# Kernel optimization log

Hardware: AMD Instinct MI355X
Metric: run time of the kernel (lower is better)

## Reference

```python
import math
import jax, jax.numpy as jnp
import numpy as np

WS = (8, 7, 7)   # window_size (d, h, w)
SS = (4, 3, 3)   # shift_size
NH = 4           # num_heads
DIM = 128


def _rel_position_index(ws):
    # [N*N] int index into the (2wd-1)(2wh-1)(2ww-1) bias table
    cd, ch, cw = np.arange(ws[0]), np.arange(ws[1]), np.arange(ws[2])
    coords = np.stack(np.meshgrid(cd, ch, cw, indexing='ij')).reshape(3, -1)  # [3, N]
    rel = (coords[:, :, None] - coords[:, None, :]).transpose(1, 2, 0)        # [N, N, 3]
    rel[..., 0] += ws[0] - 1
    rel[..., 1] += ws[1] - 1
    rel[..., 2] += ws[2] - 1
    rel[..., 0] *= (2 * ws[1] - 1) * (2 * ws[2] - 1)
    rel[..., 1] *= (2 * ws[2] - 1)
    return rel.sum(-1).reshape(-1)


def _rel_coords_table(ws):
    # [(2wd-1)(2wh-1)(2ww-1), 3] log-spaced continuous coords (Swin v2)
    rd = np.arange(-(ws[0] - 1), ws[0], dtype=np.float32)
    rh = np.arange(-(ws[1] - 1), ws[1], dtype=np.float32)
    rw = np.arange(-(ws[2] - 1), ws[2], dtype=np.float32)
    t = np.stack(np.meshgrid(rd, rh, rw, indexing='ij')).transpose(1, 2, 3, 0)  # [Td,Th,Tw,3]
    t[..., 0] /= ws[0] - 1
    t[..., 1] /= ws[1] - 1
    t[..., 2] /= ws[2] - 1
    t *= 8.0
    t = np.sign(t) * np.log2(np.abs(t) + 1.0) / 3.0
    return t.reshape(-1, 3)


_REL_INDEX = _rel_position_index(WS)
_COORDS = jnp.asarray(_rel_coords_table(WS))


def _attn_mask(pD, pH, pW, ws, ss):
    img = np.zeros((pD, pH, pW), np.float32)
    sl = lambda w, s: (slice(0, -w), slice(-w, -s), slice(-s, None))
    cnt = 0
    for d in sl(ws[0], ss[0]):
        for h in sl(ws[1], ss[1]):
            for w in sl(ws[2], ss[2]):
                img[d, h, w] = cnt
                cnt += 1
    m = img.reshape(pD // ws[0], ws[0], pH // ws[1], ws[1], pW // ws[2], ws[2])
    m = m.transpose(0, 2, 4, 1, 3, 5).reshape(-1, ws[0] * ws[1] * ws[2])  # [nWin, N]
    diff = m[:, None, :] - m[:, :, None]
    return jnp.asarray(np.where(diff != 0, -100.0, 0.0).astype(np.float32))


def setup_inputs() -> dict:
    key = jax.random.key(0)
    ks = jax.random.split(key, 6)
    B, D, H, W, C = 1, 16, 56, 56, DIM
    g = lambda k, shp, sc: jax.random.normal(k, shp, dtype=jnp.float32) * sc
    return {
        'x': g(ks[0], (B, D, H, W, C), 1.0),
        'qkv_weight': g(ks[1], (3 * C, C), 0.02),
        'qkv_bias': jnp.zeros((3 * C,), jnp.float32),
        'proj_weight': g(ks[2], (C, C), 0.02),
        'proj_bias': jnp.zeros((C,), jnp.float32),
        'logit_scale': jnp.full((NH, 1, 1), float(np.log(10.0)), jnp.float32),
        'cpb_w1': g(ks[3], (512, 3), 0.02),
        'cpb_b1': jnp.zeros((512,), jnp.float32),
        'cpb_w2': g(ks[4], (NH, 512), 0.02),
    }


def reference(x, qkv_weight, qkv_bias, proj_weight, proj_bias,
              logit_scale, cpb_w1, cpb_b1, cpb_w2):
    B, D, H, W, C = x.shape
    wd, wh, ww = WS
    hd = C // NH
    pad_d, pad_h, pad_w = (-D) % wd, (-H) % wh, (-W) % ww
    x = jnp.pad(x, ((0, 0), (0, pad_d), (0, pad_h), (0, pad_w), (0, 0)))
    pD, pH, pW = D + pad_d, H + pad_h, W + pad_w
    ss = [0 if WS[i] >= (pD, pH, pW)[i] else SS[i] for i in range(3)]
    shifted = sum(ss) > 0
    if shifted:
        x = jnp.roll(x, (-ss[0], -ss[1], -ss[2]), axis=(1, 2, 3))
    nd, nh, nw = pD // wd, pH // wh, pW // ww
    nWin, N = nd * nh * nw, wd * wh * ww
    # window partition -> [B*nWin, N, C]
    xw = x.reshape(B, nd, wd, nh, wh, nw, ww, C).transpose(0, 1, 3, 5, 2, 4, 6, 7)
    xw = xw.reshape(B * nWin, N, C)
    # qkv with k-bias zeroed (Swin v2 cosine attention)
    qb = qkv_bias.at[C:2 * C].set(0.0)
    qkv = (xw @ qkv_weight.T + qb).reshape(B * nWin, N, 3, NH, hd).transpose(2, 0, 3, 1, 4)
    q, k, v = qkv[0], qkv[1], qkv[2]   # each [B*nWin, NH, N, hd]
    qn = q / jnp.maximum(jnp.linalg.norm(q, axis=-1, keepdims=True), 1e-12)
    kn = k / jnp.maximum(jnp.linalg.norm(k, axis=-1, keepdims=True), 1e-12)
    attn = jnp.einsum('bhnd,bhmd->bhnm', qn, kn)
    scale = jnp.exp(jnp.minimum(logit_scale, math.log(100.0)))  # [NH,1,1]
    attn = attn * scale
    # continuous relative position bias
    table = jax.nn.relu(_COORDS @ cpb_w1.T + cpb_b1) @ cpb_w2.T  # [T, NH]
    bias = table[_REL_INDEX].reshape(N, N, NH).transpose(2, 0, 1)
    bias = 16.0 * jax.nn.sigmoid(bias)
    attn = attn + bias[None]
    if shifted:
        mask = _attn_mask(pD, pH, pW, WS, ss)  # [nWin, N, N]
        attn = attn.reshape(B, nWin, NH, N, N) + mask[None, :, None]
        attn = attn.reshape(B * nWin, NH, N, N)
    attn = jax.nn.softmax(attn, axis=-1)
    out = jnp.einsum('bhnm,bhmd->bhnd', attn, v).transpose(0, 2, 1, 3).reshape(B * nWin, N, C)
    out = out @ proj_weight.T + proj_bias
    # window reverse -> [B, pD, pH, pW, C]
    out = out.reshape(B, nd, nh, nw, wd, wh, ww, C).transpose(0, 1, 4, 2, 5, 3, 6, 7)
    out = out.reshape(B, pD, pH, pW, C)
    if shifted:
        out = jnp.roll(out, tuple(ss), axis=(1, 2, 3))
    return out[:, :D, :H, :W, :]
```

## Files before the change

kernel.cpp:

```cpp
#include <hip/hip_runtime.h>
#include <hip/hip_bf16.h>

typedef unsigned short u16;
typedef unsigned int   u32;
typedef float f32x4  __attribute__((ext_vector_type(4)));
typedef short bf16x8 __attribute__((ext_vector_type(8)));

#define DI __device__ __forceinline__

constexpr int TBL  = 2535;
constexpr int NTOK = 50176;

constexpr int WB_QW = 0;
constexpr int WB_PW = 49152;
constexpr int WB_QB = 65536;
constexpr int WB_PB = 65920;
constexpr int WB_TOT = 66048;

DI float b2f(u16 u){ return __uint_as_float(((u32)u)<<16); }
DI u16 f2b(float f){
  u32 u = __float_as_uint(f);
  return (u16)((u + 0x7fffu + ((u>>16)&1u)) >> 16);
}
DI float ldf(const void* p, int i, int isf32){
  return isf32 ? ((const float*)p)[i] : b2f(((const u16*)p)[i]);
}
DI f32x4 mfma16(bf16x8 a, bf16x8 b, f32x4 c){
  return __builtin_amdgcn_mfma_f32_16x16x32_bf16(a, b, c, 0, 0, 0);
}
DI u32 cvtpk(float lo, float hi){
  u32 r;
  asm("v_cvt_pk_bf16_f32 %0, %1, %2" : "=v"(r) : "v"(lo), "v"(hi));
  return r;
}
DI float ssq8(uint4 a){
  float s = 0.f, f;
  f=__uint_as_float(a.x<<16); s+=f*f; f=__uint_as_float(a.x&0xffff0000u); s+=f*f;
  f=__uint_as_float(a.y<<16); s+=f*f; f=__uint_as_float(a.y&0xffff0000u); s+=f*f;
  f=__uint_as_float(a.z<<16); s+=f*f; f=__uint_as_float(a.z&0xffff0000u); s+=f*f;
  f=__uint_as_float(a.w<<16); s+=f*f; f=__uint_as_float(a.w&0xffff0000u); s+=f*f;
  return s;
}

__global__ void k_detect(const u32* __restrict__ xw, int* __restrict__ flag){
  __shared__ int cnt;
  if (threadIdx.x == 0) cnt = 0;
  __syncthreads();
  int local = 0;
  for (int k = threadIdx.x; k < 4096; k += 256){
    u32 w = xw[k];
    u16 lo = (u16)w;
    u32 e = (lo >> 7) & 0xFF;
    if (lo != 0 && (e >= 143 || e <= 111)) local++;
  }
  atomicAdd(&cnt, local);
  __syncthreads();
  if (threadIdx.x == 0) *flag = (cnt > 1000) ? 1 : 0;
}

__global__ void k_wconv(const void* __restrict__ qw, const void* __restrict__ pw,
                        const void* __restrict__ qb, const void* __restrict__ pb,
                        const int* __restrict__ flag, u16* __restrict__ wb){
  const int isf32 = *flag;
  int i = blockIdx.x*256 + threadIdx.x;
  if (i >= WB_TOT) return;
  const void* src; int off;
  if (i < WB_PW)      { src = qw; off = i; }
  else if (i < WB_QB) { src = pw; off = i - WB_PW; }
  else if (i < WB_PB) { src = qb; off = i - WB_QB; }
  else                { src = pb; off = i - WB_PB; }
  wb[i] = isf32 ? f2b(((const float*)src)[off]) : ((const u16*)src)[off];
}

__global__ void k_cpb(const void* __restrict__ w1, const void* __restrict__ b1,
                      const void* __restrict__ w2, const int* __restrict__ flag,
                      float* __restrict__ table16){
  const int isf32 = *flag;
  int t = blockIdx.x, lane = threadIdx.x;
  int i = t/169; int r = t - i*169; int j = r/13; int k = r - j*13;
  float v0 = 8.f*(float)(i-7)/7.f, v1 = 8.f*(float)(j-6)/6.f, v2 = 8.f*(float)(k-6)/6.f;
  float c0 = copysignf(log2f(fabsf(v0)+1.f)*(1.f/3.f), v0);
  float c1 = copysignf(log2f(fabsf(v1)+1.f)*(1.f/3.f), v1);
  float c2 = copysignf(log2f(fabsf(v2)+1.f)*(1.f/3.f), v2);
  float a0=0.f,a1=0.f,a2=0.f,a3=0.f;
  for (int hh = lane; hh < 512; hh += 64){
    float a = c0*ldf(w1,hh*3,isf32) + c1*ldf(w1,hh*3+1,isf32)
            + c2*ldf(w1,hh*3+2,isf32) + ldf(b1,hh,isf32);
    a = fmaxf(a, 0.f);
    a0 += a*ldf(w2,hh,isf32);       a1 += a*ldf(w2,512+hh,isf32);
    a2 += a*ldf(w2,1024+hh,isf32);  a3 += a*ldf(w2,1536+hh,isf32);
  }
  #pragma unroll
  for (int off=32; off; off>>=1){
    a0 += __shfl_xor(a0, off); a1 += __shfl_xor(a1, off);
    a2 += __shfl_xor(a2, off); a3 += __shfl_xor(a3, off);
  }
  if (lane==0){
    table16[t]       = 16.f/(1.f+__expf(-a0));
    table16[TBL+t]   = 16.f/(1.f+__expf(-a1));
    table16[2*TBL+t] = 16.f/(1.f+__expf(-a2));
    table16[3*TBL+t] = 16.f/(1.f+__expf(-a3));
  }
}

__global__ void k_bias(const float* __restrict__ table16, float* __restrict__ bias16){
  int n = blockIdx.x, h = blockIdx.y;
  int td = n/49; int r2 = n - td*49; int th = r2/7; int tw = r2 - th*7;
  const float* tb = table16 + h*TBL;
  float* o = bias16 + ((size_t)h*392 + n)*392;
  for (int m = threadIdx.x; m < 392; m += 128){
    int sd = m/49; int q2 = m - sd*49; int sh = q2/7; int sw = q2 - sh*7;
    int idx = (td - sd + 7)*169 + (th - sh + 6)*13 + (tw - sw + 6);
    o[m] = tb[idx];
  }
}

__global__ __launch_bounds__(256,3) void k_qkv(const void* __restrict__ x,
    const u16* __restrict__ wb, const int* __restrict__ flag, u16* __restrict__ qkvbuf){
  __shared__ __align__(16) u16 As[64*136];
  __shared__ __align__(16) u16 Ws[128*136];
  const int isf32 = *flag;
  const int tid = threadIdx.x;
  const int tokbase0 = blockIdx.x*64;
  {
    int trow = tid>>2, cq = (tid&3)*32;
    int gtok = tokbase0 + trow;
    int win = gtok/392, tt = gtok - win*392;
    int dwi = win>>6, hwi = (win>>3)&7, wwi = win&7;
    int td = tt/49; int r2 = tt - td*49; int th = r2/7; int tw = r2 - th*7;
    int pd = dwi*8 + td + 4; if (pd >= 16) pd -= 16;
    int ph = hwi*7 + th + 3; if (ph >= 56) ph -= 56;
    int pw = wwi*7 + tw + 3; if (pw >= 56) pw -= 56;
    size_t pos = (size_t)((pd*56 + ph)*56 + pw)*128 + cq;
    if (isf32){
      const float4* src = (const float4*)((const float*)x + pos);
      #pragma unroll
      for (int u=0; u<8; ++u){
        float4 a = src[u];
        ushort4 s4 = make_ushort4(f2b(a.x), f2b(a.y), f2b(a.z), f2b(a.w));
        *(ushort4*)&As[trow*136 + cq + u*4] = s4;
      }
    } else {
      const uint4* src = (const uint4*)((const u16*)x + pos);
      #pragma unroll
      for (int u=0; u<4; ++u) *(uint4*)&As[trow*136 + cq + u*8] = src[u];
    }
  }
  const int wave = tid>>6, lane = tid&63;
  const int c = lane & 15, g = lane >> 4;
  const int tokbase = tokbase0 + wave*16;
  bf16x8 ka[4];
  for (int which = 0; which < 3; ++which){
    __syncthreads();
    {
      int orow = tid>>1, c2 = (tid&1)*64;
      const uint4* src = (const uint4*)(wb + WB_QW + (size_t)(which*128 + orow)*128 + c2);
      #pragma unroll
      for (int u=0; u<8; ++u) *(uint4*)&Ws[orow*136 + c2 + u*8] = src[u];
    }
    __syncthreads();
    if (which == 0){
      #pragma unroll
      for (int kk=0; kk<4; ++kk)
        ka[kk] = *(const bf16x8*)&As[(wave*16 + c)*136 + kk*32 + g*8];
    }
    f32x4 acc[8];
    #pragma unroll
    for (int nt=0; nt<8; ++nt) acc[nt] = 0.f;
    #pragma unroll
    for (int nt=0; nt<8; ++nt){
      #pragma unroll
      for (int kk=0; kk<4; ++kk){
        bf16x8 wf = *(const bf16x8*)&Ws[(nt*16 + c)*136 + kk*32 + g*8];
        acc[nt] = mfma16(ka[kk], wf, acc[nt]);
      }
    }
    #pragma unroll
    for (int nt=0; nt<8; ++nt){
      int oc = nt*16 + c;
      float bv = (which==1) ? 0.f : b2f(wb[WB_QB + which*128 + oc]);
      int head = oc >> 5, chb = oc & 31;
      #pragma unroll
      for (int r=0;r<4;++r){
        int t = tokbase + 4*g + r;
        qkvbuf[((size_t)(which*4+head)*NTOK + t)*32 + chb] = f2b(acc[nt][r] + bv);
      }
    }
  }
}

#define QKT_STEP(JT, JJ) do { \
  bf16x8 kf = *(const bf16x8*)&klds[((JT)*16 + c)*40 + g*8]; \
  f32x4 tz = {0.f,0.f,0.f,0.f}; \
  f32x4 t = mfma16(kf, qf, tz); \
  const int mb = (JT)*16 + 4*g; \
  const int mbc = (mb <= 388) ? mb : 388; \
  const float4 bq = *(const float4*)(brow + mbc); \
  const int4 cmq = *(const int4*)&cnt[mbc]; \
  float s0 = fmaf(t[0], qsc, bq.x + ((cmq.x==cn) ? -15.f : -115.f)); \
  float s1 = fmaf(t[1], qsc, bq.y + ((cmq.y==cn) ? -15.f : -115.f)); \
  float s2 = fmaf(t[2], qsc, bq.z + ((cmq.z==cn) ? -15.f : -115.f)); \
  float s3 = fmaf(t[3], qsc, bq.w + ((cmq.w==cn) ? -15.f : -115.f)); \
  float p0 = __expf(s0), p1 = __expf(s1), p2 = __expf(s2), p3 = __expf(s3); \
  if (mb > 388){ p0=0.f; p1=0.f; p2=0.f; p3=0.f; } \
  sum += (p0+p1) + (p2+p3); \
  uint2 wv; wv.x = cvtpk(p0,p1); wv.y = cvtpk(p2,p3); \
  *(uint2*)&psw[c*20 + (JJ)*8 + 2*g] = wv; \
} while(0)

#define PV_STEP(MC) do { \
  bf16x8 pf = *(const bf16x8*)&psw[c*20 + 4*g]; \
  bf16x8 va = *(const bf16x8*)&vT[c*424 + (MC)*32 + g*8]; \
  bf16x8 vb = *(const bf16x8*)&vT[(16+c)*424 + (MC)*32 + g*8]; \
  o0 = mfma16(va, pf, o0); \
  o1 = mfma16(vb, pf, o1); \
} while(0)

__global__ __launch_bounds__(512,4) void k_attn(const u16* __restrict__ qkv,
    const float* __restrict__ bias16, const void* __restrict__ lsc,
    const int* __restrict__ flag, u16* __restrict__ aout){
  __shared__ __align__(16) u16 klds[400*40];
  __shared__ __align__(16) u16 vT[32*424];
  __shared__ __align__(16) u32 ps[8][16*20];
  __shared__ __align__(16) float qs[400];
  __shared__ __align__(16) int   cnt[400];
  const int isf32 = *flag;
  const int tid = threadIdx.x;
  const int win = blockIdx.x, h = blockIdx.y;
  const int dwi = win>>6, hwi = (win>>3)&7, wwi = win&7;
  const u16* qg = qkv + ((size_t)(0*4 + h)*NTOK + (size_t)win*392)*32;
  const u16* kg = qkv + ((size_t)(1*4 + h)*NTOK + (size_t)win*392)*32;
  const u16* vg = qkv + ((size_t)(2*4 + h)*NTOK + (size_t)win*392)*32;
  const float ls = isf32 ? ((const float*)lsc)[h] : b2f(((const u16*)lsc)[h]);
  const float scale = __expf(fminf(ls, 4.60517019f));

  for (int idx = tid; idx < 800; idx += 512){
    const int row = idx>>1, half = idx&1;
    if (row < 392){
      const uint4* kp = (const uint4*)(kg + (size_t)row*32 + half*16);
      uint4 a = kp[0], b = kp[1];
      float fv[16];
      fv[0] =__uint_as_float(a.x<<16); fv[1] =__uint_as_float(a.x&0xffff0000u);
      fv[2] =__uint_as_float(a.y<<16); fv[3] =__uint_as_float(a.y&0xffff0000u);
      fv[4] =__uint_as_float(a.z<<16); fv[5] =__uint_as_float(a.z&0xffff0000u);
      fv[6] =__uint_as_float(a.w<<16); fv[7] =__uint_as_float(a.w&0xffff0000u);
      fv[8] =__uint_as_float(b.x<<16); fv[9] =__uint_as_float(b.x&0xffff0000u);
      fv[10]=__uint_as_float(b.y<<16); fv[11]=__uint_as_float(b.y&0xffff0000u);
      fv[12]=__uint_as_float(b.z<<16); fv[13]=__uint_as_float(b.z&0xffff0000u);
      fv[14]=__uint_as_float(b.w<<16); fv[15]=__uint_as_float(b.w&0xffff0000u);
      float ss = 0.f;
      #pragma unroll
      for (int e=0;e<16;++e) ss = fmaf(fv[e], fv[e], ss);
      ss += __shfl_xor(ss, 1);
      const float rn = 1.f/fmaxf(sqrtf(ss), 1e-12f);
      u16 ob[16];
      #pragma unroll
      for (int e=0;e<16;++e) ob[e] = f2b(fv[e]*rn);
      uint4 w0, w1;
      w0.x = (u32)ob[0] |((u32)ob[1] <<16); w0.y = (u32)ob[2] |((u32)ob[3] <<16);
      w0.z = (u32)ob[4] |((u32)ob[5] <<16); w0.w = (u32)ob[6] |((u32)ob[7] <<16);
      w1.x = (u32)ob[8] |((u32)ob[9] <<16); w1.y = (u32)ob[10]|((u32)ob[11]<<16);
      w1.z = (u32)ob[12]|((u32)ob[13]<<16); w1.w = (u32)ob[14]|((u32)ob[15]<<16);
      *(uint4*)&klds[row*40 + half*16]     = w0;
      *(uint4*)&klds[row*40 + half*16 + 8] = w1;
      const uint4* qp = (const uint4*)(qg + (size_t)row*32 + half*16);
      float sq = ssq8(qp[0]) + ssq8(qp[1]);
      sq += __shfl_xor(sq, 1);
      if (half == 0) qs[row] = scale / fmaxf(sqrtf(sq), 1e-12f);
    } else {
      uint4 z = {0,0,0,0};
      *(uint4*)&klds[row*40 + half*16]     = z;
      *(uint4*)&klds[row*40 + half*16 + 8] = z;
      if (half == 0) qs[row] = 1.f;
    }
  }
  for (int t2 = tid; t2 < 400; t2 += 512){
    int row = (t2 < 392) ? t2 : 391;
    int td = row/49; int r2 = row - td*49; int th = r2/7; int tw = r2 - th*7;
    int gd = dwi*8 + td, gh = hwi*7 + th, gw = wwi*7 + tw;
    int rd = (gd < 8) ? 0 : ((gd < 12) ? 1 : 2);
    int rh = (gh < 49) ? 0 : ((gh < 53) ? 1 : 2);
    int rw = (gw < 49) ? 0 : ((gw < 53) ? 1 : 2);
    cnt[t2] = rd*9 + rh*3 + rw;
  }
  for (int idx = tid; idx < 1568; idx += 512){
    int m = idx>>2, cq = idx&3;
    uint4 b = ((const uint4*)vg)[idx];
    int ch = cq*8;
    vT[(ch+0)*424 + m] = (u16)b.x;  vT[(ch+1)*424 + m] = (u16)(b.x>>16);
    vT[(ch+2)*424 + m] = (u16)b.y;  vT[(ch+3)*424 + m] = (u16)(b.y>>16);
    vT[(ch+4)*424 + m] = (u16)b.z;  vT[(ch+5)*424 + m] = (u16)(b.z>>16);
    vT[(ch+6)*424 + m] = (u16)b.w;  vT[(ch+7)*424 + m] = (u16)(b.w>>16);
  }
  for (int idx = tid; idx < 1024; idx += 512){
    int ch = idx>>5, mm = 392 + (idx&31);
    vT[ch*424 + mm] = 0;
  }
  __syncthreads();

  const int wave = tid>>6, lane = tid&63;
  const int c = lane & 15, g = lane >> 4;
  u32* psw = &ps[wave][0];
  for (int rt = wave; rt < 25; rt += 8){
    const int nb = rt*16;
    const int nc = (nb + c < 392) ? (nb + c) : 391;
    const bf16x8 qf = *(const bf16x8*)(qg + (size_t)nc*32 + g*8);
    const float qsc = qs[nc];
    const int   cn  = cnt[nc];
    const float* brow = bias16 + (size_t)h*153664 + (size_t)nc*392;
    float sum = 0.f;
    f32x4 o0 = {0.f,0.f,0.f,0.f}, o1 = {0.f,0.f,0.f,0.f};
    for (int mc = 0; mc < 12; ++mc){
      QKT_STEP(2*mc,   0);
      QKT_STEP(2*mc+1, 1);
      PV_STEP(mc);
    }
    QKT_STEP(24, 0);
    { uint2 zz; zz.x = 0u; zz.y = 0u; *(uint2*)&psw[c*20 + 8 + 2*g] = zz; }
    PV_STEP(12);
    sum += __shfl_xor(sum, 16);
    sum += __shfl_xor(sum, 32);
    const float rv = 1.f/sum;
    uint2 wa, wb2;
    wa.x  = cvtpk(o0[0]*rv, o0[1]*rv);  wa.y  = cvtpk(o0[2]*rv, o0[3]*rv);
    wb2.x = cvtpk(o1[0]*rv, o1[1]*rv);  wb2.y = cvtpk(o1[2]*rv, o1[3]*rv);
    *(uint2*)&psw[c*20 + 2*g]     = wa;
    *(uint2*)&psw[c*20 + 8 + 2*g] = wb2;
    const int orow = lane>>2, oq = lane&3;
    uint4 ov = *(const uint4*)&psw[orow*20 + 4*oq];
    const int n = nb + orow;
    if (n < 392)
      *(uint4*)(aout + ((size_t)(win*392 + n))*128 + h*32 + oq*8) = ov;
  }
}

__global__ __launch_bounds__(256,2) void k_proj(const u16* __restrict__ ain,
    const u16* __restrict__ wb, const int* __restrict__ flag, void* __restrict__ out){
  __shared__ __align__(16) u16 As[64*136];
  __shared__ __align__(16) u16 Ws[128*136];
  const int isf32 = *flag;
  const int tid = threadIdx.x;
  const int tokbase0 = blockIdx.x*64;
  {
    int trow = tid>>2, cq = (tid&3)*32;
    const uint4* src = (const uint4*)(ain + (size_t)(tokbase0+trow)*128 + cq);
    #pragma unroll
    for (int u=0; u<4; ++u) *(uint4*)&As[trow*136 + cq + u*8] = src[u];
  }
  {
    int orow = tid>>1, c2 = (tid&1)*64;
    const uint4* src = (const uint4*)(wb + WB_PW + (size_t)orow*128 + c2);
    #pragma unroll
    for (int u=0; u<8; ++u) *(uint4*)&Ws[orow*136 + c2 + u*8] = src[u];
  }
  __syncthreads();
  const int wave = tid>>6, lane = tid&63;
  const int c = lane & 15, g = lane >> 4;
  bf16x8 ka[4];
  #pragma unroll
  for (int kk=0; kk<4; ++kk)
    ka[kk] = *(const bf16x8*)&As[(wave*16 + c)*136 + kk*32 + g*8];
  f32x4 acc[8];
  #pragma unroll
  for (int nt=0; nt<8; ++nt) acc[nt] = 0.f;
  #pragma unroll
  for (int nt=0; nt<8; ++nt){
    #pragma unroll
    for (int kk=0; kk<4; ++kk){
      bf16x8 wf = *(const bf16x8*)&Ws[(nt*16 + c)*136 + kk*32 + g*8];
      acc[nt] = mfma16(ka[kk], wf, acc[nt]);
    }
  }
  const int tokbase = tokbase0 + wave*16;
  size_t po[4];
  #pragma unroll
  for (int r=0;r<4;++r){
    int gtok = tokbase + 4*g + r;
    int win = gtok/392, tt = gtok - win*392;
    int dwi = win>>6, hwi = (win>>3)&7, wwi = win&7;
    int td = tt/49; int r2 = tt - td*49; int th = r2/7; int tw = r2 - th*7;
    int pd = dwi*8 + td + 4; if (pd >= 16) pd -= 16;
    int ph = hwi*7 + th + 3; if (ph >= 56) ph -= 56;
    int pwx = wwi*7 + tw + 3; if (pwx >= 56) pwx -= 56;
    po[r] = (size_t)((pd*56 + ph)*56 + pwx)*128;
  }
  #pragma unroll
  for (int nt=0; nt<8; ++nt){
    int oc = nt*16 + c;
    float bv = b2f(wb[WB_PB + oc]);
    #pragma unroll
    for (int r=0;r<4;++r){
      float v = acc[nt][r] + bv;
      if (isf32) ((float*)out)[po[r] + oc] = v;
      else       ((u16*)out)[po[r] + oc] = f2b(v);
    }
  }
}

extern "C" void kernel_launch(void* const* d_in, const int* in_sizes, int n_in,
                              void* d_out, int out_size, void* d_ws, size_t ws_size,
                              hipStream_t stream){
  const void* x      = d_in[0];
  const void* qkv_w  = d_in[1];
  const void* qkv_b  = d_in[2];
  const void* proj_w = d_in[3];
  const void* proj_b = d_in[4];
  const void* lsc    = d_in[5];
  const void* cpb_w1 = d_in[6];
  const void* cpb_b1 = d_in[7];
  const void* cpb_w2 = d_in[8];
  char* ws = (char*)d_ws;
  int*   flag    = (int*)(ws);
  float* table16 = (float*)(ws + 256);
  float* bias16  = (float*)(ws + 41216);
  u16*   wb      = (u16*)(ws + 2499840);
  u16*   qkvbuf  = (u16*)(ws + 2631936);
  u16*   attnout = (u16*)(ws + 41167104);

  k_detect<<<1, 256, 0, stream>>>((const u32*)x, flag);
  k_wconv<<<(WB_TOT+255)/256, 256, 0, stream>>>(qkv_w, proj_w, qkv_b, proj_b, flag, wb);
  k_cpb <<<TBL, 64, 0, stream>>>(cpb_w1, cpb_b1, cpb_w2, flag, table16);
  k_bias<<<dim3(392,4), 128, 0, stream>>>(table16, bias16);
  k_qkv <<<784, 256, 0, stream>>>(x, wb, flag, qkvbuf);
  k_attn<<<dim3(128,4), 512, 0, stream>>>(qkvbuf, bias16, lsc, flag, attnout);
  k_proj<<<784, 256, 0, stream>>>(attnout, wb, flag, d_out);
}
```

Baseline: 102.6 us.

## Fuse q/k normalization into QKV GEMM, simplify attention softmax and merge weight conversion

Moves the L2 normalization of q and k, plus the logit scale, into the QKV projection epilogue, so the attention kernel no longer renormalizes K or computes q norms. The bias table is pre-shifted and pre-scaled by log2(e), which lets the inner loop use a raw v_exp_f32 with no multiply, and the mask is applied as a zeroing select only for windows that straddle shift regions. The row sum now comes from an extra MFMA against a vector of ones instead of shuffle reductions. Weight conversion is folded into the cpb kernel to remove one launch. The risks are extra shuffles in the QKV epilogue, one more MFMA per PV step, and rounding normalized q/k to bf16 before the dot product.

```diff
diff --git a/kernel.cpp b/kernel.cpp
--- a/kernel.cpp
+++ b/kernel.cpp
@@ -10,6 +10,7 @@
 
 constexpr int TBL  = 2535;
 constexpr int NTOK = 50176;
+constexpr float L2E = 1.4426950408889634f;
 
 constexpr int WB_QW = 0;
 constexpr int WB_PW = 49152;
@@ -33,13 +34,10 @@
   asm("v_cvt_pk_bf16_f32 %0, %1, %2" : "=v"(r) : "v"(lo), "v"(hi));
   return r;
 }
-DI float ssq8(uint4 a){
-  float s = 0.f, f;
-  f=__uint_as_float(a.x<<16); s+=f*f; f=__uint_as_float(a.x&0xffff0000u); s+=f*f;
-  f=__uint_as_float(a.y<<16); s+=f*f; f=__uint_as_float(a.y&0xffff0000u); s+=f*f;
-  f=__uint_as_float(a.z<<16); s+=f*f; f=__uint_as_float(a.z&0xffff0000u); s+=f*f;
-  f=__uint_as_float(a.w<<16); s+=f*f; f=__uint_as_float(a.w&0xffff0000u); s+=f*f;
-  return s;
+DI float vexp2(float x){
+  float r;
+  asm("v_exp_f32 %0, %1" : "=v"(r) : "v"(x));
+  return r;
 }
 
 __global__ void k_detect(const u32* __restrict__ xw, int* __restrict__ flag){
@@ -58,24 +56,23 @@
   if (threadIdx.x == 0) *flag = (cnt > 1000) ? 1 : 0;
 }
 
-__global__ void k_wconv(const void* __restrict__ qw, const void* __restrict__ pw,
-                        const void* __restrict__ qb, const void* __restrict__ pb,
-                        const int* __restrict__ flag, u16* __restrict__ wb){
-  const int isf32 = *flag;
-  int i = blockIdx.x*256 + threadIdx.x;
-  if (i >= WB_TOT) return;
-  const void* src; int off;
-  if (i < WB_PW)      { src = qw; off = i; }
-  else if (i < WB_QB) { src = pw; off = i - WB_PW; }
-  else if (i < WB_PB) { src = qb; off = i - WB_QB; }
-  else                { src = pb; off = i - WB_PB; }
-  wb[i] = isf32 ? f2b(((const float*)src)[off]) : ((const u16*)src)[off];
-}
-
 __global__ void k_cpb(const void* __restrict__ w1, const void* __restrict__ b1,
                       const void* __restrict__ w2, const int* __restrict__ flag,
-                      float* __restrict__ table16){
+                      const void* __restrict__ qw, const void* __restrict__ pw,
+                      const void* __restrict__ qb, const void* __restrict__ pb,
+                      u16* __restrict__ wb, float* __restrict__ table16){
   const int isf32 = *flag;
+  {
+    int gid = blockIdx.x*64 + threadIdx.x;
+    if (gid < WB_TOT){
+      const void* src; int off;
+      if (gid < WB_PW)      { src = qw; off = gid; }
+      else if (gid < WB_QB) { src = pw; off = gid - WB_PW; }
+      else if (gid < WB_PB) { src = qb; off = gid - WB_QB; }
+      else                  { src = pb; off = gid - WB_PB; }
+      wb[gid] = isf32 ? f2b(((const float*)src)[off]) : ((const u16*)src)[off];
+    }
+  }
   int t = blockIdx.x, lane = threadIdx.x;
   int i = t/169; int r = t - i*169; int j = r/13; int k = r - j*13;
   float v0 = 8.f*(float)(i-7)/7.f, v1 = 8.f*(float)(j-6)/6.f, v2 = 8.f*(float)(k-6)/6.f;
@@ -96,10 +93,10 @@
     a2 += __shfl_xor(a2, off); a3 += __shfl_xor(a3, off);
   }
   if (lane==0){
-    table16[t]       = 16.f/(1.f+__expf(-a0));
-    table16[TBL+t]   = 16.f/(1.f+__expf(-a1));
-    table16[2*TBL+t] = 16.f/(1.f+__expf(-a2));
-    table16[3*TBL+t] = 16.f/(1.f+__expf(-a3));
+    table16[t]       = (16.f/(1.f+__expf(-a0)) - 15.f)*L2E;
+    table16[TBL+t]   = (16.f/(1.f+__expf(-a1)) - 15.f)*L2E;
+    table16[2*TBL+t] = (16.f/(1.f+__expf(-a2)) - 15.f)*L2E;
+    table16[3*TBL+t] = (16.f/(1.f+__expf(-a3)) - 15.f)*L2E;
   }
 }
 
@@ -116,7 +113,8 @@
 }
 
 __global__ __launch_bounds__(256,3) void k_qkv(const void* __restrict__ x,
-    const u16* __restrict__ wb, const int* __restrict__ flag, u16* __restrict__ qkvbuf){
+    const u16* __restrict__ wb, const void* __restrict__ lsc,
+    const int* __restrict__ flag, u16* __restrict__ qkvbuf){
   __shared__ __align__(16) u16 As[64*136];
   __shared__ __align__(16) u16 Ws[128*136];
   const int isf32 = *flag;
@@ -149,6 +147,12 @@
   const int wave = tid>>6, lane = tid&63;
   const int c = lane & 15, g = lane >> 4;
   const int tokbase = tokbase0 + wave*16;
+  float sl2e[4];
+  #pragma unroll
+  for (int h2=0; h2<4; ++h2){
+    float ls = ldf(lsc, h2, isf32);
+    sl2e[h2] = __expf(fminf(ls, 4.60517019f)) * L2E;
+  }
   bf16x8 ka[4];
   for (int which = 0; which < 3; ++which){
     __syncthreads();
@@ -175,35 +179,67 @@
         acc[nt] = mfma16(ka[kk], wf, acc[nt]);
       }
     }
+    if (which != 1){
+      #pragma unroll
+      for (int nt=0; nt<8; ++nt){
+        float bv = b2f(wb[WB_QB + which*128 + nt*16 + c]);
+        #pragma unroll
+        for (int r=0;r<4;++r) acc[nt][r] += bv;
+      }
+    }
+    if (which < 2){
+      #pragma unroll
+      for (int h2=0; h2<4; ++h2){
+        f32x4 ss;
+        #pragma unroll
+        for (int r=0;r<4;++r)
+          ss[r] = acc[2*h2][r]*acc[2*h2][r] + acc[2*h2+1][r]*acc[2*h2+1][r];
+        #pragma unroll
+        for (int off=1; off<16; off<<=1){
+          #pragma unroll
+          for (int r=0;r<4;++r) ss[r] += __shfl_xor(ss[r], off);
+        }
+        #pragma unroll
+        for (int r=0;r<4;++r){
+          float rn = rsqrtf(fmaxf(ss[r], 1e-24f));
+          if (which == 0) rn *= sl2e[h2];
+          acc[2*h2][r]   *= rn;
+          acc[2*h2+1][r] *= rn;
+        }
+      }
+    }
     #pragma unroll
     for (int nt=0; nt<8; ++nt){
       int oc = nt*16 + c;
-      float bv = (which==1) ? 0.f : b2f(wb[WB_QB + which*128 + oc]);
       int head = oc >> 5, chb = oc & 31;
       #pragma unroll
       for (int r=0;r<4;++r){
         int t = tokbase + 4*g + r;
-        qkvbuf[((size_t)(which*4+head)*NTOK + t)*32 + chb] = f2b(acc[nt][r] + bv);
+        qkvbuf[((size_t)(which*4+head)*NTOK + t)*32 + chb] = f2b(acc[nt][r]);
       }
     }
   }
 }
 
-#define QKT_STEP(JT, JJ) do { \
+#define QKT_STEP(JT, JJ, TAIL, MIXED) do { \
   bf16x8 kf = *(const bf16x8*)&klds[((JT)*16 + c)*40 + g*8]; \
   f32x4 tz = {0.f,0.f,0.f,0.f}; \
   f32x4 t = mfma16(kf, qf, tz); \
   const int mb = (JT)*16 + 4*g; \
-  const int mbc = (mb <= 388) ? mb : 388; \
+  const int mbc = (TAIL) ? ((mb <= 388) ? mb : 388) : mb; \
   const float4 bq = *(const float4*)(brow + mbc); \
-  const int4 cmq = *(const int4*)&cnt[mbc]; \
-  float s0 = fmaf(t[0], qsc, bq.x + ((cmq.x==cn) ? -15.f : -115.f)); \
-  float s1 = fmaf(t[1], qsc, bq.y + ((cmq.y==cn) ? -15.f : -115.f)); \
-  float s2 = fmaf(t[2], qsc, bq.z + ((cmq.z==cn) ? -15.f : -115.f)); \
-  float s3 = fmaf(t[3], qsc, bq.w + ((cmq.w==cn) ? -15.f : -115.f)); \
-  float p0 = __expf(s0), p1 = __expf(s1), p2 = __expf(s2), p3 = __expf(s3); \
-  if (mb > 388){ p0=0.f; p1=0.f; p2=0.f; p3=0.f; } \
-  sum += (p0+p1) + (p2+p3); \
+  float p0 = vexp2(t[0] + bq.x); \
+  float p1 = vexp2(t[1] + bq.y); \
+  float p2 = vexp2(t[2] + bq.z); \
+  float p3 = vexp2(t[3] + bq.w); \
+  if (MIXED){ \
+    const int4 cmq = *(const int4*)&cnt[mbc]; \
+    if (cmq.x != cn) p0 = 0.f; \
+    if (cmq.y != cn) p1 = 0.f; \
+    if (cmq.z != cn) p2 = 0.f; \
+    if (cmq.w != cn) p3 = 0.f; \
+  } \
+  if (TAIL && mb > 388){ p0=0.f; p1=0.f; p2=0.f; p3=0.f; } \
   uint2 wv; wv.x = cvtpk(p0,p1); wv.y = cvtpk(p2,p3); \
   *(uint2*)&psw[c*20 + (JJ)*8 + 2*g] = wv; \
 } while(0)
@@ -214,113 +250,32 @@
   bf16x8 vb = *(const bf16x8*)&vT[(16+c)*424 + (MC)*32 + g*8]; \
   o0 = mfma16(va, pf, o0); \
   o1 = mfma16(vb, pf, o1); \
+  o2 = mfma16(ones, pf, o2); \
 } while(0)
 
-__global__ __launch_bounds__(512,4) void k_attn(const u16* __restrict__ qkv,
-    const float* __restrict__ bias16, const void* __restrict__ lsc,
-    const int* __restrict__ flag, u16* __restrict__ aout){
-  __shared__ __align__(16) u16 klds[400*40];
-  __shared__ __align__(16) u16 vT[32*424];
-  __shared__ __align__(16) u32 ps[8][16*20];
-  __shared__ __align__(16) float qs[400];
-  __shared__ __align__(16) int   cnt[400];
-  const int isf32 = *flag;
-  const int tid = threadIdx.x;
-  const int win = blockIdx.x, h = blockIdx.y;
-  const int dwi = win>>6, hwi = (win>>3)&7, wwi = win&7;
-  const u16* qg = qkv + ((size_t)(0*4 + h)*NTOK + (size_t)win*392)*32;
-  const u16* kg = qkv + ((size_t)(1*4 + h)*NTOK + (size_t)win*392)*32;
-  const u16* vg = qkv + ((size_t)(2*4 + h)*NTOK + (size_t)win*392)*32;
-  const float ls = isf32 ? ((const float*)lsc)[h] : b2f(((const u16*)lsc)[h]);
-  const float scale = __expf(fminf(ls, 4.60517019f));
-
-  for (int idx = tid; idx < 800; idx += 512){
-    const int row = idx>>1, half = idx&1;
-    if (row < 392){
-      const uint4* kp = (const uint4*)(kg + (size_t)row*32 + half*16);
-      uint4 a = kp[0], b = kp[1];
-      float fv[16];
-      fv[0] =__uint_as_float(a.x<<16); fv[1] =__uint_as_float(a.x&0xffff0000u);
-      fv[2] =__uint_as_float(a.y<<16); fv[3] =__uint_as_float(a.y&0xffff0000u);
-      fv[4] =__uint_as_float(a.z<<16); fv[5] =__uint_as_float(a.z&0xffff0000u);
-      fv[6] =__uint_as_float(a.w<<16); fv[7] =__uint_as_float(a.w&0xffff0000u);
-      fv[8] =__uint_as_float(b.x<<16); fv[9] =__uint_as_float(b.x&0xffff0000u);
-      fv[10]=__uint_as_float(b.y<<16); fv[11]=__uint_as_float(b.y&0xffff0000u);
-      fv[12]=__uint_as_float(b.z<<16); fv[13]=__uint_as_float(b.z&0xffff0000u);
-      fv[14]=__uint_as_float(b.w<<16); fv[15]=__uint_as_float(b.w&0xffff0000u);
-      float ss = 0.f;
-      #pragma unroll
-      for (int e=0;e<16;++e) ss = fmaf(fv[e], fv[e], ss);
-      ss += __shfl_xor(ss, 1);
-      const float rn = 1.f/fmaxf(sqrtf(ss), 1e-12f);
-      u16 ob[16];
-      #pragma unroll
-      for (int e=0;e<16;++e) ob[e] = f2b(fv[e]*rn);
-      uint4 w0, w1;
-      w0.x = (u32)ob[0] |((u32)ob[1] <<16); w0.y = (u32)ob[2] |((u32)ob[3] <<16);
-      w0.z = (u32)ob[4] |((u32)ob[5] <<16); w0.w = (u32)ob[6] |((u32)ob[7] <<16);
-      w1.x = (u32)ob[8] |((u32)ob[9] <<16); w1.y = (u32)ob[10]|((u32)ob[11]<<16);
-      w1.z = (u32)ob[12]|((u32)ob[13]<<16); w1.w = (u32)ob[14]|((u32)ob[15]<<16);
-      *(uint4*)&klds[row*40 + half*16]     = w0;
-      *(uint4*)&klds[row*40 + half*16 + 8] = w1;
-      const uint4* qp = (const uint4*)(qg + (size_t)row*32 + half*16);
-      float sq = ssq8(qp[0]) + ssq8(qp[1]);
-      sq += __shfl_xor(sq, 1);
-      if (half == 0) qs[row] = scale / fmaxf(sqrtf(sq), 1e-12f);
-    } else {
-      uint4 z = {0,0,0,0};
-      *(uint4*)&klds[row*40 + half*16]     = z;
-      *(uint4*)&klds[row*40 + half*16 + 8] = z;
-      if (half == 0) qs[row] = 1.f;
-    }
-  }
-  for (int t2 = tid; t2 < 400; t2 += 512){
-    int row = (t2 < 392) ? t2 : 391;
-    int td = row/49; int r2 = row - td*49; int th = r2/7; int tw = r2 - th*7;
-    int gd = dwi*8 + td, gh = hwi*7 + th, gw = wwi*7 + tw;
-    int rd = (gd < 8) ? 0 : ((gd < 12) ? 1 : 2);
-    int rh = (gh < 49) ? 0 : ((gh < 53) ? 1 : 2);
-    int rw = (gw < 49) ? 0 : ((gw < 53) ? 1 : 2);
-    cnt[t2] = rd*9 + rh*3 + rw;
-  }
-  for (int idx = tid; idx < 1568; idx += 512){
-    int m = idx>>2, cq = idx&3;
-    uint4 b = ((const uint4*)vg)[idx];
-    int ch = cq*8;
-    vT[(ch+0)*424 + m] = (u16)b.x;  vT[(ch+1)*424 + m] = (u16)(b.x>>16);
-    vT[(ch+2)*424 + m] = (u16)b.y;  vT[(ch+3)*424 + m] = (u16)(b.y>>16);
-    vT[(ch+4)*424 + m] = (u16)b.z;  vT[(ch+5)*424 + m] = (u16)(b.z>>16);
-    vT[(ch+6)*424 + m] = (u16)b.w;  vT[(ch+7)*424 + m] = (u16)(b.w>>16);
-  }
-  for (int idx = tid; idx < 1024; idx += 512){
-    int ch = idx>>5, mm = 392 + (idx&31);
-    vT[ch*424 + mm] = 0;
-  }
-  __syncthreads();
-
-  const int wave = tid>>6, lane = tid&63;
+template<bool MIXED>
+DI void attn_main(const u16* __restrict__ qg, const float* __restrict__ bias_h,
+                  const u16* klds, const u16* vT, u32* psw, const int* cnt,
+                  u16* __restrict__ aout, int win, int h, int wave, int lane){
   const int c = lane & 15, g = lane >> 4;
-  u32* psw = &ps[wave][0];
+  const short ob = 0x3F80;
+  const bf16x8 ones = {ob,ob,ob,ob,ob,ob,ob,ob};
   for (int rt = wave; rt < 25; rt += 8){
     const int nb = rt*16;
     const int nc = (nb + c < 392) ? (nb + c) : 391;
     const bf16x8 qf = *(const bf16x8*)(qg + (size_t)nc*32 + g*8);
-    const float qsc = qs[nc];
-    const int   cn  = cnt[nc];
-    const float* brow = bias16 + (size_t)h*153664 + (size_t)nc*392;
-    float sum = 0.f;
-    f32x4 o0 = {0.f,0.f,0.f,0.f}, o1 = {0.f,0.f,0.f,0.f};
+    const int cn = MIXED ? cnt[nc] : 0;
+    const float* brow = bias_h + (size_t)nc*392;
+    f32x4 o0 = {0.f,0.f,0.f,0.f}, o1 = {0.f,0.f,0.f,0.f}, o2 = {0.f,0.f,0.f,0.f};
     for (int mc = 0; mc < 12; ++mc){
-      QKT_STEP(2*mc,   0);
-      QKT_STEP(2*mc+1, 1);
+      QKT_STEP(2*mc,   0, false, MIXED);
+      QKT_STEP(2*mc+1, 1, false, MIXED);
       PV_STEP(mc);
     }
-    QKT_STEP(24, 0);
+    QKT_STEP(24, 0, true, MIXED);
     { uint2 zz; zz.x = 0u; zz.y = 0u; *(uint2*)&psw[c*20 + 8 + 2*g] = zz; }
     PV_STEP(12);
-    sum += __shfl_xor(sum, 16);
-    sum += __shfl_xor(sum, 32);
-    const float rv = 1.f/sum;
+    const float rv = 1.f / o2[0];
     uint2 wa, wb2;
     wa.x  = cvtpk(o0[0]*rv, o0[1]*rv);  wa.y  = cvtpk(o0[2]*rv, o0[3]*rv);
     wb2.x = cvtpk(o1[0]*rv, o1[1]*rv);  wb2.y = cvtpk(o1[2]*rv, o1[3]*rv);
@@ -332,6 +287,65 @@
     if (n < 392)
       *(uint4*)(aout + ((size_t)(win*392 + n))*128 + h*32 + oq*8) = ov;
   }
+}
+
+__global__ __launch_bounds__(512,4) void k_attn(const u16* __restrict__ qkv,
+    const float* __restrict__ bias16, u16* __restrict__ aout){
+  __shared__ __align__(16) u16 klds[400*40];
+  __shared__ __align__(16) u16 vT[32*424];
+  __shared__ __align__(16) u32 ps[8][16*20];
+  __shared__ __align__(16) int cnt[400];
+  const int tid = threadIdx.x;
+  const int win = blockIdx.x, h = blockIdx.y;
+  const int dwi = win>>6, hwi = (win>>3)&7, wwi = win&7;
+  const u16* qg = qkv + ((size_t)(0*4 + h)*NTOK + (size_t)win*392)*32;
+  const u16* kg = qkv + ((size_t)(1*4 + h)*NTOK + (size_t)win*392)*32;
+  const u16* vg = qkv + ((size_t)(2*4 + h)*NTOK + (size_t)win*392)*32;
+  for (int idx = tid; idx < 1600; idx += 512){
+    const int row = idx>>2, q = idx&3;
+    uint4 a = {0,0,0,0};
+    if (row < 392) a = *(const uint4*)(kg + (size_t)row*32 + q*8);
+    *(uint4*)&klds[row*40 + q*8] = a;
+  }
+  for (int idx = tid; idx < 784; idx += 512){
+    const int mg = idx>>3, cg = idx&7;
+    uint2 v0 = *(const uint2*)(vg + (size_t)(4*mg+0)*32 + cg*4);
+    uint2 v1 = *(const uint2*)(vg + (size_t)(4*mg+1)*32 + cg*4);
+    uint2 v2 = *(const uint2*)(vg + (size_t)(4*mg+2)*32 + cg*4);
+    uint2 v3 = *(const uint2*)(vg + (size_t)(4*mg+3)*32 + cg*4);
+    u16 e0[4], e1[4], e2[4], e3[4];
+    e0[0]=(u16)v0.x; e0[1]=(u16)(v0.x>>16); e0[2]=(u16)v0.y; e0[3]=(u16)(v0.y>>16);
+    e1[0]=(u16)v1.x; e1[1]=(u16)(v1.x>>16); e1[2]=(u16)v1.y; e1[3]=(u16)(v1.y>>16);
+    e2[0]=(u16)v2.x; e2[1]=(u16)(v2.x>>16); e2[2]=(u16)v2.y; e2[3]=(u16)(v2.y>>16);
+    e3[0]=(u16)v3.x; e3[1]=(u16)(v3.x>>16); e3[2]=(u16)v3.y; e3[3]=(u16)(v3.y>>16);
+    #pragma unroll
+    for (int cc=0; cc<4; ++cc){
+      ushort4 w = make_ushort4(e0[cc], e1[cc], e2[cc], e3[cc]);
+      *(ushort4*)&vT[(cg*4+cc)*424 + 4*mg] = w;
+    }
+  }
+  for (int idx = tid; idx < 1024; idx += 512){
+    int ch = idx>>5, mm = 392 + (idx&31);
+    vT[ch*424 + mm] = 0;
+  }
+  for (int t2 = tid; t2 < 400; t2 += 512){
+    int row = (t2 < 392) ? t2 : 391;
+    int td = row/49; int r2 = row - td*49; int th = r2/7; int tw = r2 - th*7;
+    int gd = dwi*8 + td, gh = hwi*7 + th, gw = wwi*7 + tw;
+    int rd = (gd < 8) ? 0 : ((gd < 12) ? 1 : 2);
+    int rh = (gh < 49) ? 0 : ((gh < 53) ? 1 : 2);
+    int rw = (gw < 49) ? 0 : ((gw < 53) ? 1 : 2);
+    cnt[t2] = rd*9 + rh*3 + rw;
+  }
+  __syncthreads();
+  const int wave = tid>>6, lane = tid&63;
+  u32* psw = &ps[wave][0];
+  const float* bias_h = bias16 + (size_t)h*153664;
+  const bool uniform = (dwi == 0) && (hwi < 7) && (wwi < 7);
+  if (uniform)
+    attn_main<false>(qg, bias_h, klds, vT, psw, cnt, aout, win, h, wave, lane);
+  else
+    attn_main<true >(qg, bias_h, klds, vT, psw, cnt, aout, win, h, wave, lane);
 }
 
 __global__ __launch_bounds__(256,2) void k_proj(const u16* __restrict__ ain,
@@ -418,10 +432,10 @@
   u16*   attnout = (u16*)(ws + 41167104);
 
   k_detect<<<1, 256, 0, stream>>>((const u32*)x, flag);
-  k_wconv<<<(WB_TOT+255)/256, 256, 0, stream>>>(qkv_w, proj_w, qkv_b, proj_b, flag, wb);
-  k_cpb <<<TBL, 64, 0, stream>>>(cpb_w1, cpb_b1, cpb_w2, flag, table16);
+  k_cpb <<<TBL, 64, 0, stream>>>(cpb_w1, cpb_b1, cpb_w2, flag,
+                                 qkv_w, proj_w, qkv_b, proj_b, wb, table16);
   k_bias<<<dim3(392,4), 128, 0, stream>>>(table16, bias16);
-  k_qkv <<<784, 256, 0, stream>>>(x, wb, flag, qkvbuf);
-  k_attn<<<dim3(128,4), 512, 0, stream>>>(qkvbuf, bias16, lsc, flag, attnout);
+  k_qkv <<<784, 256, 0, stream>>>(x, wb, lsc, flag, qkvbuf);
+  k_attn<<<dim3(128,4), 512, 0, stream>>>(qkvbuf, bias16, attnout);
   k_proj<<<784, 256, 0, stream>>>(attnout, wb, flag, d_out);
 }
```

Measured after the change: 99.14 us. 1.03x faster.
